# Optimization experiments

Measured on AMD Instinct MI355X. Metric: run time of the kernel, lower is better.

## Reference

```python
import jax, jax.numpy as jnp
import numpy as np

N_NODES = 1000
HIDDEN = 256
IN_DIM = 128
N_EDGES = 64000


def setup_inputs() -> dict:
    key = jax.random.key(0)
    ks = jax.random.split(key, 24)
    inp = {
        "x": jax.random.normal(ks[0], (N_NODES, IN_DIM), dtype=jnp.float32),
        "edge_index": jax.random.randint(ks[1], (2, N_EDGES), 0, N_NODES, dtype=jnp.int64),
    }
    dims = [(HIDDEN, 2 * IN_DIM)] + [(HIDDEN, 2 * HIDDEN)] * 4
    for l, (dout, din) in enumerate(dims):
        s0 = 1.0 / np.sqrt(din)
        s1 = 1.0 / np.sqrt(HIDDEN)
        inp[f"w{l}_0"] = jax.random.normal(ks[2 + 4 * l], (dout, din), dtype=jnp.float32) * s0
        inp[f"b{l}_0"] = jax.random.normal(ks[3 + 4 * l], (dout,), dtype=jnp.float32) * s0
        inp[f"w{l}_1"] = jax.random.normal(ks[4 + 4 * l], (HIDDEN, HIDDEN), dtype=jnp.float32) * s1
        inp[f"b{l}_1"] = jax.random.normal(ks[5 + 4 * l], (HIDDEN,), dtype=jnp.float32) * s1
    return inp


def _edge_conv(x, src, dst, w1, b1, w2, b2):
    # gather endpoint features per edge: [E, D]
    x_i = x[dst]  # destination (edge_index[1])
    x_j = x[src]  # source (edge_index[0])
    m = jnp.concatenate([x_i, x_j - x_i], axis=-1)  # [E, 2D]
    h = jax.nn.relu(m @ w1.T + b1) @ w2.T + b2      # 2-layer MLP, [E, HIDDEN]
    # scatter-max to destination nodes (include_self=False -> empty rows = 0)
    agg = jax.ops.segment_max(h, dst, num_segments=N_NODES)
    agg = jnp.where(jnp.isneginf(agg), jnp.zeros((), agg.dtype), agg)
    return jax.nn.relu(agg)


def reference(x, edge_index, w0_0, b0_0, w0_1, b0_1, w1_0, b1_0, w1_1, b1_1,
              w2_0, b2_0, w2_1, b2_1, w3_0, b3_0, w3_1, b3_1, w4_0, b4_0, w4_1, b4_1):
    src = edge_index[0]
    dst = edge_index[1]
    params = [(w0_0, b0_0, w0_1, b0_1), (w1_0, b1_0, w1_1, b1_1),
              (w2_0, b2_0, w2_1, b2_1), (w3_0, b3_0, w3_1, b3_1),
              (w4_0, b4_0, w4_1, b4_1)]
    h = x
    for (w1, b1, w2, b2) in params:
        h = _edge_conv(h, src, dst, w1, b1, w2, b2)
    return h
```

## Files before the change

### kernel.cpp

```cpp
#include <hip/hip_runtime.h>

#define NN 1000
#define NE 64000
#define HH 256

typedef _Float16 half8 __attribute__((ext_vector_type(8)));
typedef float floatx4 __attribute__((ext_vector_type(4)));

struct PrepArgs { const float* w0[5]; const float* w1[5]; };


__global__ __launch_bounds__(256) void k_prep(PrepArgs pa,
                                              _Float16* wnode, _Float16* w2h,
                                              int* counts, int* cursor,
                                              float* aggA) {
    int gtid = blockIdx.x * 256 + threadIdx.x;
    int gstride = gridDim.x * 256;
    for (int i = gtid; i < 1024; i += gstride) { counts[i] = 0; cursor[i] = 0; }
    for (int l = 0; l < 5; l++) {
        const int KK = l ? 8 : 4;
        const int D = KK * 32;
        const int lgKK = l ? 3 : 2;
        const float* w0 = pa.w0[l];
        _Float16* wn = wnode + l * 131072;
        for (int i = gtid; i < 16384 * KK; i += gstride) {
            int j = i & 7;
            int lane = (i >> 3) & 63;
            int nt = (i >> 9) & 1;
            int kk = (i >> 10) & (KK - 1);
            int slice = i >> (10 + lgKK);
            int mn = lane & 15, q = lane >> 4;
            int n = slice * 32 + nt * 16 + mn;
            int k = kk * 32 + q * 8 + j;
            float v = (n < 256) ? (w0[n * 2 * D + k] - w0[n * 2 * D + D + k])
                                : w0[(n - 256) * 2 * D + D + k];
            wn[i] = (_Float16)v;
        }
        const float* w1 = pa.w1[l];
        _Float16* w2 = w2h + l * 65536;
        for (int i = gtid; i < 65536; i += gstride) {
            int j = i & 7;
            int lane = (i >> 3) & 63;
            int nt = (i >> 9) & 3;
            int kk = (i >> 11) & 7;
            int ws = (i >> 14) & 3;
            int mn = lane & 15, q = lane >> 4;
            int row = ws * 64 + nt * 16 + mn;
            int col = kk * 32 + q * 8 + j;
            w2[i] = (_Float16)w1[row * 256 + col];
        }
    }
    floatx4 z = {0.f, 0.f, 0.f, 0.f};
    floatx4* p4 = (floatx4*)aggA;
    for (int i = gtid; i < NN * HH / 4; i += gstride) p4[i] = z;
}

template <int NK>
__device__ __forceinline__ void node_tile(const float* __restrict__ X,
                                          const _Float16* __restrict__ Wn,
                                          const float* __restrict__ b0,
                                          _Float16* __restrict__ out, int bid) {
    const int Kd = NK * 32;
    int t = threadIdx.x;
    int wave = t >> 6, lane = t & 63;
    int q = lane >> 4, mn = lane & 15;
    int m0 = (bid % 63) * 16;
    int n0 = (bid / 63) * 128 + wave * 32;
    int slice = (bid / 63) * 4 + wave;
    int rr = m0 + mn;
    if (rr >= NN) rr = NN - 1;

    half8 afa[NK];
    half8 bfa[NK][2];
#pragma unroll
    for (int kk = 0; kk < NK; kk++) {
        int ka = kk * 32 + q * 8;
        const float* p = X + (size_t)rr * Kd + ka;
        floatx4 x0 = *(const floatx4*)p;
        floatx4 x1 = *(const floatx4*)(p + 4);
        half8 aa;
#pragma unroll
        for (int j = 0; j < 4; j++) { aa[j] = (_Float16)x0[j]; aa[4 + j] = (_Float16)x1[j]; }
        afa[kk] = aa;
        bfa[kk][0] = *(const half8*)(Wn + (((slice * NK + kk) * 2 + 0) * 64 + lane) * 8);
        bfa[kk][1] = *(const half8*)(Wn + (((slice * NK + kk) * 2 + 1) * 64 + lane) * 8);
    }
    floatx4 acc[2] = {};
#pragma unroll
    for (int kk = 0; kk < NK; kk++) {
        acc[0] = __builtin_amdgcn_mfma_f32_16x16x32_f16(afa[kk], bfa[kk][0], acc[0], 0, 0, 0);
        acc[1] = __builtin_amdgcn_mfma_f32_16x16x32_f16(afa[kk], bfa[kk][1], acc[1], 0, 0, 0);
    }
#pragma unroll
    for (int nt = 0; nt < 2; nt++) {
        int col = n0 + nt * 16 + mn;
        float bias = (col < 256) ? b0[col] : 0.f;
#pragma unroll
        for (int r2 = 0; r2 < 4; r2++) {
            int orow = m0 + q * 4 + r2;
            if (orow < NN)
                out[(size_t)orow * 512 + col] = (_Float16)(acc[nt][r2] + bias);
        }
    }
}

__global__ __launch_bounds__(256) void k_hist_node0(const int* __restrict__ ei,
                                                    int* __restrict__ counts,
                                                    const float* __restrict__ X,
                                                    const _Float16* __restrict__ Wn,
                                                    const float* __restrict__ b0,
                                                    _Float16* __restrict__ out) {
    int bid = blockIdx.x;
    if (bid < 4) {
        for (int e = bid * 256 + threadIdx.x; e < NE; e += 4 * 256)
            atomicAdd(&counts[ei[NE + e] & 1023], 1);
    } else {
        node_tile<4>(X, Wn, b0, out, bid - 4);
    }
}

__global__ __launch_bounds__(256) void k_scatter2(const int* __restrict__ ei,
                                                  const int* __restrict__ counts,
                                                  int* __restrict__ cursor,
                                                  int* __restrict__ ssrc,
                                                  int* __restrict__ sdst) {
    __shared__ int sbase[1024];
    __shared__ int ssum[256];
    int t = threadIdx.x;
    int base = t * 4;
    int c4[4]; int sum = 0;
#pragma unroll
    for (int j = 0; j < 4; j++) { c4[j] = counts[base + j]; sum += c4[j]; }
    ssum[t] = sum;
    __syncthreads();
    for (int d = 1; d < 256; d <<= 1) {
        int v = (t >= d) ? ssum[t - d] : 0;
        __syncthreads();
        ssum[t] += v;
        __syncthreads();
    }
    int run = (t > 0) ? ssum[t - 1] : 0;
#pragma unroll
    for (int j = 0; j < 4; j++) { sbase[base + j] = run; run += c4[j]; }
    __syncthreads();
    for (int e = blockIdx.x * 256 + t; e < NE; e += gridDim.x * 256) {
        int s = ei[e] & 1023, d = ei[NE + e] & 1023;
        int pos = sbase[d] + atomicAdd(&cursor[d], 1);
        if (pos < NE) { ssrc[pos] = s; sdst[pos] = d; }
    }
}

__global__ __launch_bounds__(256) void k_node_zero(const float* __restrict__ agg_in,
                                                   const _Float16* __restrict__ Wn,
                                                   const float* __restrict__ b0,
                                                   _Float16* __restrict__ out,
                                                   float* __restrict__ agg_next) {
    int bid = blockIdx.x;
    if (bid < 252) {
        node_tile<8>(agg_in, Wn, b0, out, bid);
    } else {
        floatx4 z = {0.f, 0.f, 0.f, 0.f};
        floatx4* p4 = (floatx4*)agg_next;
        for (int i = (bid - 252) * 256 + (int)threadIdx.x; i < NN * HH / 4; i += 64 * 256)
            p4[i] = z;
    }
}

template <bool LAST>
__global__ __launch_bounds__(256, 4) void edge_gemm2(const _Float16* __restrict__ node_ab,
                          const int* __restrict__ ssrc, const int* __restrict__ sdst,
                          const _Float16* __restrict__ W2, const float* __restrict__ b2,
                          float* __restrict__ agg) {
    __shared__ _Float16 h1[64 * 256];
    __shared__ int sd[64];
    int t = threadIdx.x;
    int e0 = blockIdx.x * 64;
    int wave = t >> 6, lane = t & 63;
    int q = lane >> 4, mn = lane & 15;
    int n0 = wave * 64;
    const _Float16* W2w = W2 + wave * 16384;

    if (t < 64) sd[t] = sdst[e0 + t];
    {
        int row = t & 63;
        int cb = (t >> 6) * 8;
        int dn = sdst[e0 + row], sn = ssrc[e0 + row];
        const _Float16* pa = node_ab + (size_t)dn * 512 + cb * 8;
        const _Float16* pb = node_ab + (size_t)sn * 512 + 256 + cb * 8;
        half8 av[8], bv[8];
#pragma unroll
        for (int i = 0; i < 8; i++) av[i] = *(const half8*)(pa + i * 8);
#pragma unroll
        for (int i = 0; i < 8; i++) bv[i] = *(const half8*)(pb + i * 8);
#pragma unroll
        for (int i = 0; i < 8; i++) {
            int c = cb + i;
            int p = (c & ~7) | ((c ^ row) & 7);
            half8 hv = av[i] + bv[i];
#pragma unroll
            for (int j = 0; j < 8; j++) hv[j] = hv[j] > (_Float16)0 ? hv[j] : (_Float16)0;
            *(half8*)(&h1[row * 256 + p * 8]) = hv;
        }
    }
    __syncthreads();

    floatx4 acc[4][4] = {};
#pragma unroll
    for (int kk = 0; kk < 8; kk++) {
        half8 bf[4];
#pragma unroll
        for (int nt = 0; nt < 4; nt++)
            bf[nt] = *(const half8*)(W2w + (kk * 4 + nt) * 512 + lane * 8);
        half8 af[4];
#pragma unroll
        for (int mt = 0; mt < 4; mt++) {
            int r = mt * 16 + mn;
            int c = kk * 4 + q;
            int p = (c & ~7) | ((c ^ r) & 7);
            af[mt] = *(const half8*)(&h1[r * 256 + p * 8]);
        }
#pragma unroll
        for (int mt = 0; mt < 4; mt++)
#pragma unroll
            for (int nt = 0; nt < 4; nt++)
                acc[mt][nt] = __builtin_amdgcn_mfma_f32_16x16x32_f16(af[mt], bf[nt], acc[mt][nt], 0, 0, 0);
    }

    if (LAST) {
#pragma unroll
        for (int nt = 0; nt < 4; nt++) {
            int col = n0 + nt * 16 + mn;
            float bias = b2[col];
            int curd = -1;
            float curv = 0.f;
#pragma unroll
            for (int mt = 0; mt < 4; mt++) {
#pragma unroll
                for (int r2 = 0; r2 < 4; r2++) {
                    int er = mt * 16 + q * 4 + r2;
                    int d = sd[er];
                    float v = acc[mt][nt][r2] + bias;
                    v = v > 0.f ? v : 0.f;
                    if (d != curd) {
                        if (curd >= 0 && curv > 0.f)
                            atomicMax((unsigned int*)(agg + (size_t)curd * HH + col), __float_as_uint(curv));
                        curd = d;
                        curv = v;
                    } else {
                        curv = fmaxf(curv, v);
                    }
                }
            }
            if (curd >= 0 && curv > 0.f)
                atomicMax((unsigned int*)(agg + (size_t)curd * HH + col), __float_as_uint(curv));
        }
        return;
    }

    __syncthreads();
#pragma unroll
    for (int nt = 0; nt < 4; nt++) {
        int col = n0 + nt * 16 + mn;
        float bias = b2[col];
        int g = col >> 3, o = col & 7;
#pragma unroll
        for (int mt = 0; mt < 4; mt++) {
#pragma unroll
            for (int r2 = 0; r2 < 4; r2++) {
                int row = mt * 16 + q * 4 + r2;
                float v = acc[mt][nt][r2] + bias;
                v = v > 0.f ? v : 0.f;
                int pg = (g & ~7) | ((g ^ row) & 7);
                h1[row * 256 + pg * 8 + o] = (_Float16)v;
            }
        }
    }
    __syncthreads();

    {
        int c = t;
        int g = c >> 3, o = c & 7;
        float* aggc = agg + c;
        float m = (float)h1[g * 8 + o];
        bool sedge = true;
        int prevd = sd[0];
#pragma unroll 8
        for (int r = 1; r < 64; r++) {
            int d = sd[r];
            int pg = (g & ~7) | ((g ^ r) & 7);
            float v = (float)h1[r * 256 + pg * 8 + o];
            if (d != prevd) {
                if (sedge) {
                    if (m > 0.f)
                        atomicMax((unsigned int*)(aggc + (size_t)prevd * HH), __float_as_uint(m));
                } else {
                    if (m > 0.f)
                        aggc[(size_t)prevd * HH] = m;
                }
                m = v; sedge = false; prevd = d;
            } else {
                m = fmaxf(m, v);
            }
        }
        if (m > 0.f)
            atomicMax((unsigned int*)(aggc + (size_t)prevd * HH), __float_as_uint(m));
    }
}

extern "C" void kernel_launch(void* const* d_in, const int* in_sizes, int n_in,
                              void* d_out, int out_size, void* d_ws, size_t ws_size,
                              hipStream_t stream) {
    const float* x = (const float*)d_in[0];
    const int* ei = (const int*)d_in[1];
    PrepArgs pa;
    const float* b0s[5];
    const float* b1s[5];
    for (int l = 0; l < 5; l++) {
        pa.w0[l] = (const float*)d_in[2 + 4 * l];
        b0s[l] = (const float*)d_in[3 + 4 * l];
        pa.w1[l] = (const float*)d_in[4 + 4 * l];
        b1s[l] = (const float*)d_in[5 + 4 * l];
    }

    int* ssrc = (int*)d_ws;
    int* sdst = ssrc + NE;
    int* counts = sdst + NE;
    int* cursor = counts + 1024;
    _Float16* node_ab = (_Float16*)(cursor + 1024);
    float* aggA = (float*)(node_ab + 1024 * 512);
    float* aggB = aggA + NN * HH;
    _Float16* wnode = (_Float16*)(aggB + NN * HH);
    _Float16* w2h = wnode + 5 * 131072;

    hipLaunchKernelGGL(k_prep, dim3(256), dim3(256), 0, stream,
                       pa, wnode, w2h, counts, cursor, aggA);
    hipLaunchKernelGGL(k_hist_node0, dim3(256), dim3(256), 0, stream,
                       ei, counts, x, wnode, b0s[0], node_ab);
    hipLaunchKernelGGL(k_scatter2, dim3(NE / 256), dim3(256), 0, stream,
                       ei, counts, cursor, ssrc, sdst);

    float* aggs[5] = {aggA, aggB, aggA, aggB, (float*)d_out};
    for (int l = 0; l < 4; l++) {
        hipLaunchKernelGGL((edge_gemm2<false>), dim3(NE / 64), dim3(256), 0, stream,
                           node_ab, ssrc, sdst, w2h + (size_t)l * 65536, b1s[l], aggs[l]);
        hipLaunchKernelGGL(k_node_zero, dim3(252 + 64), dim3(256), 0, stream,
                           aggs[l], wnode + (size_t)(l + 1) * 131072, b0s[l + 1],
                           node_ab, aggs[l + 1]);
    }
    hipLaunchKernelGGL((edge_gemm2<true>), dim3(NE / 64), dim3(256), 0, stream,
                       node_ab, ssrc, sdst, w2h + (size_t)4 * 65536, b1s[4], (float*)d_out);
}
```

Measured before the change: 279.0 us.

## Fuse edge and node stages into single kernels with grid-wide atomic barriers

Merges the histogram, node GEMM and scatter into one kernel, and merges each layer's edge GEMM, zeroing and next-layer node GEMM into one kernel, using software grid barriers on atomic counters in place of kernel boundaries. This removes several launches and their idle gaps. The last layer gets a new reduction path that stages fp32 values in padded shared memory instead of per-lane atomics. The barriers rely on all 1000 blocks being co-resident, which risks deadlock if occupancy is not met. Node tiles now write into node_ab while other blocks in the same kernel may still be reading it.

After: 720.0 us. +158.0%, slower.

```diff
diff --git a/kernel.cpp b/kernel.cpp
--- a/kernel.cpp
+++ b/kernel.cpp
@@ -13,10 +13,10 @@
 __global__ __launch_bounds__(256) void k_prep(PrepArgs pa,
                                               _Float16* wnode, _Float16* w2h,
                                               int* counts, int* cursor,
-                                              float* aggA) {
+                                              int* dcnt, float* aggA) {
     int gtid = blockIdx.x * 256 + threadIdx.x;
     int gstride = gridDim.x * 256;
-    for (int i = gtid; i < 1024; i += gstride) { counts[i] = 0; cursor[i] = 0; }
+    for (int i = gtid; i < 1024; i += gstride) { counts[i] = 0; cursor[i] = 0; dcnt[i] = 0; }
     for (int l = 0; l < 5; l++) {
         const int KK = l ? 8 : 4;
         const int D = KK * 32;
@@ -59,7 +59,7 @@
 __device__ __forceinline__ void node_tile(const float* __restrict__ X,
                                           const _Float16* __restrict__ Wn,
                                           const float* __restrict__ b0,
-                                          _Float16* __restrict__ out, int bid) {
+                                          _Float16* out, int bid) {
     const int Kd = NK * 32;
     int t = threadIdx.x;
     int wave = t >> 6, lane = t & 63;
@@ -69,9 +69,7 @@
     int slice = (bid / 63) * 4 + wave;
     int rr = m0 + mn;
     if (rr >= NN) rr = NN - 1;
-
-    half8 afa[NK];
-    half8 bfa[NK][2];
+    floatx4 acc[2] = {};
 #pragma unroll
     for (int kk = 0; kk < NK; kk++) {
         int ka = kk * 32 + q * 8;
@@ -81,15 +79,10 @@
         half8 aa;
 #pragma unroll
         for (int j = 0; j < 4; j++) { aa[j] = (_Float16)x0[j]; aa[4 + j] = (_Float16)x1[j]; }
-        afa[kk] = aa;
-        bfa[kk][0] = *(const half8*)(Wn + (((slice * NK + kk) * 2 + 0) * 64 + lane) * 8);
-        bfa[kk][1] = *(const half8*)(Wn + (((slice * NK + kk) * 2 + 1) * 64 + lane) * 8);
-    }
-    floatx4 acc[2] = {};
-#pragma unroll
-    for (int kk = 0; kk < NK; kk++) {
-        acc[0] = __builtin_amdgcn_mfma_f32_16x16x32_f16(afa[kk], bfa[kk][0], acc[0], 0, 0, 0);
-        acc[1] = __builtin_amdgcn_mfma_f32_16x16x32_f16(afa[kk], bfa[kk][1], acc[1], 0, 0, 0);
+        half8 bf0 = *(const half8*)(Wn + (((slice * NK + kk) * 2 + 0) * 64 + lane) * 8);
+        half8 bf1 = *(const half8*)(Wn + (((slice * NK + kk) * 2 + 1) * 64 + lane) * 8);
+        acc[0] = __builtin_amdgcn_mfma_f32_16x16x32_f16(aa, bf0, acc[0], 0, 0, 0);
+        acc[1] = __builtin_amdgcn_mfma_f32_16x16x32_f16(aa, bf1, acc[1], 0, 0, 0);
     }
 #pragma unroll
     for (int nt = 0; nt < 2; nt++) {
@@ -104,29 +97,43 @@
     }
 }
 
-__global__ __launch_bounds__(256) void k_hist_node0(const int* __restrict__ ei,
-                                                    int* __restrict__ counts,
-                                                    const float* __restrict__ X,
-                                                    const _Float16* __restrict__ Wn,
-                                                    const float* __restrict__ b0,
-                                                    _Float16* __restrict__ out) {
-    int bid = blockIdx.x;
+__device__ __forceinline__ void barrier_arrive(int* dcnt) {
+    __threadfence();
+    __syncthreads();
+    if (threadIdx.x == 0)
+        __hip_atomic_fetch_add(dcnt, 1, __ATOMIC_ACQ_REL, __HIP_MEMORY_SCOPE_AGENT);
+}
+
+__device__ __forceinline__ void barrier_wait(int* dcnt, int target) {
+    if (threadIdx.x == 0)
+        while (__hip_atomic_load(dcnt, __ATOMIC_RELAXED, __HIP_MEMORY_SCOPE_AGENT) < target)
+            __builtin_amdgcn_s_sleep(1);
+    __syncthreads();
+    __threadfence();
+}
+
+__global__ __launch_bounds__(256) void k_pre(const int* __restrict__ ei,
+                                             int* __restrict__ counts,
+                                             int* __restrict__ cursor,
+                                             const float* __restrict__ X,
+                                             const _Float16* __restrict__ Wn,
+                                             const float* __restrict__ b0,
+                                             _Float16* nab,
+                                             int* __restrict__ ssrc,
+                                             int* __restrict__ sdst,
+                                             int* dcnt) {
+    __shared__ int sbase[1024];
+    __shared__ int ssum[256];
+    int bid = blockIdx.x, t = threadIdx.x;
     if (bid < 4) {
-        for (int e = bid * 256 + threadIdx.x; e < NE; e += 4 * 256)
+        for (int e = bid * 256 + t; e < NE; e += 4 * 256)
             atomicAdd(&counts[ei[NE + e] & 1023], 1);
     } else {
-        node_tile<4>(X, Wn, b0, out, bid - 4);
-    }
-}
-
-__global__ __launch_bounds__(256) void k_scatter2(const int* __restrict__ ei,
-                                                  const int* __restrict__ counts,
-                                                  int* __restrict__ cursor,
-                                                  int* __restrict__ ssrc,
-                                                  int* __restrict__ sdst) {
-    __shared__ int sbase[1024];
-    __shared__ int ssum[256];
-    int t = threadIdx.x;
+        node_tile<4>(X, Wn, b0, nab, bid - 4);
+    }
+    barrier_arrive(dcnt);
+    barrier_wait(dcnt, 256);
+
     int base = t * 4;
     int c4[4]; int sum = 0;
 #pragma unroll
@@ -143,41 +150,23 @@
 #pragma unroll
     for (int j = 0; j < 4; j++) { sbase[base + j] = run; run += c4[j]; }
     __syncthreads();
-    for (int e = blockIdx.x * 256 + t; e < NE; e += gridDim.x * 256) {
+    for (int e = bid * 256 + t; e < NE; e += gridDim.x * 256) {
         int s = ei[e] & 1023, d = ei[NE + e] & 1023;
         int pos = sbase[d] + atomicAdd(&cursor[d], 1);
         if (pos < NE) { ssrc[pos] = s; sdst[pos] = d; }
     }
 }
 
-__global__ __launch_bounds__(256) void k_node_zero(const float* __restrict__ agg_in,
-                                                   const _Float16* __restrict__ Wn,
-                                                   const float* __restrict__ b0,
-                                                   _Float16* __restrict__ out,
-                                                   float* __restrict__ agg_next) {
-    int bid = blockIdx.x;
-    if (bid < 252) {
-        node_tile<8>(agg_in, Wn, b0, out, bid);
-    } else {
-        floatx4 z = {0.f, 0.f, 0.f, 0.f};
-        floatx4* p4 = (floatx4*)agg_next;
-        for (int i = (bid - 252) * 256 + (int)threadIdx.x; i < NN * HH / 4; i += 64 * 256)
-            p4[i] = z;
-    }
-}
-
-template <bool LAST>
-__global__ __launch_bounds__(256, 4) void edge_gemm2(const _Float16* __restrict__ node_ab,
-                          const int* __restrict__ ssrc, const int* __restrict__ sdst,
-                          const _Float16* __restrict__ W2, const float* __restrict__ b2,
-                          float* __restrict__ agg) {
-    __shared__ _Float16 h1[64 * 256];
-    __shared__ int sd[64];
+__device__ __forceinline__ void edge_mfma(const _Float16* node_ab,
+                                          const int* __restrict__ ssrc,
+                                          const int* __restrict__ sdst,
+                                          const _Float16* __restrict__ W2,
+                                          int tile, _Float16* h1, int* sd,
+                                          floatx4 acc[4][4]) {
     int t = threadIdx.x;
-    int e0 = blockIdx.x * 64;
+    int e0 = tile * 64;
     int wave = t >> 6, lane = t & 63;
     int q = lane >> 4, mn = lane & 15;
-    int n0 = wave * 64;
     const _Float16* W2w = W2 + wave * 16384;
 
     if (t < 64) sd[t] = sdst[e0 + t];
@@ -204,7 +193,6 @@
     }
     __syncthreads();
 
-    floatx4 acc[4][4] = {};
 #pragma unroll
     for (int kk = 0; kk < 8; kk++) {
         half8 bf[4];
@@ -225,42 +213,28 @@
             for (int nt = 0; nt < 4; nt++)
                 acc[mt][nt] = __builtin_amdgcn_mfma_f32_16x16x32_f16(af[mt], bf[nt], acc[mt][nt], 0, 0, 0);
     }
-
-    if (LAST) {
-#pragma unroll
-        for (int nt = 0; nt < 4; nt++) {
-            int col = n0 + nt * 16 + mn;
-            float bias = b2[col];
-            int curd = -1;
-            float curv = 0.f;
-#pragma unroll
-            for (int mt = 0; mt < 4; mt++) {
-#pragma unroll
-                for (int r2 = 0; r2 < 4; r2++) {
-                    int er = mt * 16 + q * 4 + r2;
-                    int d = sd[er];
-                    float v = acc[mt][nt][r2] + bias;
-                    v = v > 0.f ? v : 0.f;
-                    if (d != curd) {
-                        if (curd >= 0 && curv > 0.f)
-                            atomicMax((unsigned int*)(agg + (size_t)curd * HH + col), __float_as_uint(curv));
-                        curd = d;
-                        curv = v;
-                    } else {
-                        curv = fmaxf(curv, v);
-                    }
-                }
-            }
-            if (curd >= 0 && curv > 0.f)
-                atomicMax((unsigned int*)(agg + (size_t)curd * HH + col), __float_as_uint(curv));
-        }
-        return;
-    }
+}
+
+__global__ __launch_bounds__(256, 4) void k_layer(
+        const _Float16* node_ab,
+        const int* __restrict__ ssrc, const int* __restrict__ sdst,
+        const _Float16* __restrict__ W2, const float* __restrict__ b2,
+        float* __restrict__ agg, float* __restrict__ aggN,
+        const _Float16* __restrict__ WnN, const float* __restrict__ b0N,
+        int* dcnt) {
+    __shared__ _Float16 h1[64 * 256];
+    __shared__ int sd[64];
+    int bid = blockIdx.x, t = threadIdx.x;
+    int wave = t >> 6, lane = t & 63;
+    int q = lane >> 4, mn = lane & 15;
+
+    floatx4 acc[4][4] = {};
+    edge_mfma(node_ab, ssrc, sdst, W2, bid, h1, sd, acc);
 
     __syncthreads();
 #pragma unroll
     for (int nt = 0; nt < 4; nt++) {
-        int col = n0 + nt * 16 + mn;
+        int col = wave * 64 + nt * 16 + mn;
         float bias = b2[col];
         int g = col >> 3, o = col & 7;
 #pragma unroll
@@ -305,6 +279,85 @@
         if (m > 0.f)
             atomicMax((unsigned int*)(aggc + (size_t)prevd * HH), __float_as_uint(m));
     }
+
+    if (bid >= 252) {
+        floatx4 z = {0.f, 0.f, 0.f, 0.f};
+        floatx4* p4 = (floatx4*)aggN;
+        for (int i = (bid - 252) * 256 + t; i < NN * HH / 4; i += 748 * 256)
+            p4[i] = z;
+    }
+
+    barrier_arrive(dcnt);
+    if (bid < 252) {
+        barrier_wait(dcnt, 1000);
+        node_tile<8>(agg, WnN, b0N, (_Float16*)node_ab, bid);
+    }
+}
+
+__global__ __launch_bounds__(256, 4) void k_last(
+        const _Float16* __restrict__ node_ab,
+        const int* __restrict__ ssrc, const int* __restrict__ sdst,
+        const _Float16* __restrict__ W2, const float* __restrict__ b2,
+        float* __restrict__ agg) {
+    __shared__ float sf[64 * 129];
+    __shared__ int sd[64];
+    _Float16* h1 = (_Float16*)sf;
+    int t = threadIdx.x;
+    int wave = t >> 6, lane = t & 63;
+    int q = lane >> 4, mn = lane & 15;
+
+    floatx4 acc[4][4] = {};
+    edge_mfma(node_ab, ssrc, sdst, W2, blockIdx.x, h1, sd, acc);
+
+    __syncthreads();
+#pragma unroll
+    for (int p = 0; p < 2; p++) {
+        if (p) __syncthreads();
+        if ((wave >> 1) == p) {
+            int lc0 = (wave & 1) * 64;
+#pragma unroll
+            for (int nt = 0; nt < 4; nt++) {
+                int col = wave * 64 + nt * 16 + mn;
+                float bias = b2[col];
+                int lc = lc0 + nt * 16 + mn;
+#pragma unroll
+                for (int mt = 0; mt < 4; mt++) {
+#pragma unroll
+                    for (int r2 = 0; r2 < 4; r2++) {
+                        int row = mt * 16 + q * 4 + r2;
+                        float v = acc[mt][nt][r2] + bias;
+                        sf[row * 129 + lc] = v > 0.f ? v : 0.f;
+                    }
+                }
+            }
+        }
+        __syncthreads();
+        if (t < 128) {
+            float* aggc = agg + p * 128 + t;
+            float m = sf[t];
+            bool sedge = true;
+            int prevd = sd[0];
+#pragma unroll 8
+            for (int r = 1; r < 64; r++) {
+                int d = sd[r];
+                float v = sf[r * 129 + t];
+                if (d != prevd) {
+                    if (sedge) {
+                        if (m > 0.f)
+                            atomicMax((unsigned int*)(aggc + (size_t)prevd * HH), __float_as_uint(m));
+                    } else {
+                        if (m > 0.f)
+                            aggc[(size_t)prevd * HH] = m;
+                    }
+                    m = v; sedge = false; prevd = d;
+                } else {
+                    m = fmaxf(m, v);
+                }
+            }
+            if (m > 0.f)
+                atomicMax((unsigned int*)(aggc + (size_t)prevd * HH), __float_as_uint(m));
+        }
+    }
 }
 
 extern "C" void kernel_launch(void* const* d_in, const int* in_sizes, int n_in,
@@ -326,27 +379,28 @@
     int* sdst = ssrc + NE;
     int* counts = sdst + NE;
     int* cursor = counts + 1024;
-    _Float16* node_ab = (_Float16*)(cursor + 1024);
+    int* dcnt = cursor + 1024;
+    _Float16* node_ab = (_Float16*)(dcnt + 1024);
     float* aggA = (float*)(node_ab + 1024 * 512);
     float* aggB = aggA + NN * HH;
     _Float16* wnode = (_Float16*)(aggB + NN * HH);
     _Float16* w2h = wnode + 5 * 131072;
 
     hipLaunchKernelGGL(k_prep, dim3(256), dim3(256), 0, stream,
-                       pa, wnode, w2h, counts, cursor, aggA);
-    hipLaunchKernelGGL(k_hist_node0, dim3(256), dim3(256), 0, stream,
-                       ei, counts, x, wnode, b0s[0], node_ab);
-    hipLaunchKernelGGL(k_scatter2, dim3(NE / 256), dim3(256), 0, stream,
-                       ei, counts, cursor, ssrc, sdst);
+                       pa, wnode, w2h, counts, cursor, dcnt, aggA);
+    hipLaunchKernelGGL(k_pre, dim3(256), dim3(256), 0, stream,
+                       ei, counts, cursor, x, wnode, b0s[0], node_ab,
+                       ssrc, sdst, dcnt + 512);
 
     float* aggs[5] = {aggA, aggB, aggA, aggB, (float*)d_out};
     for (int l = 0; l < 4; l++) {
-        hipLaunchKernelGGL((edge_gemm2<false>), dim3(NE / 64), dim3(256), 0, stream,
-                           node_ab, ssrc, sdst, w2h + (size_t)l * 65536, b1s[l], aggs[l]);
-        hipLaunchKernelGGL(k_node_zero, dim3(252 + 64), dim3(256), 0, stream,
-                           aggs[l], wnode + (size_t)(l + 1) * 131072, b0s[l + 1],
-                           node_ab, aggs[l + 1]);
-    }
-    hipLaunchKernelGGL((edge_gemm2<true>), dim3(NE / 64), dim3(256), 0, stream,
-                       node_ab, ssrc, sdst, w2h + (size_t)4 * 65536, b1s[4], (float*)d_out);
-}
+        hipLaunchKernelGGL(k_layer, dim3(NE / 64), dim3(256), 0, stream,
+                           node_ab, ssrc, sdst, w2h + (size_t)l * 65536, b1s[l],
+                           aggs[l], aggs[l + 1],
+                           wnode + (size_t)(l + 1) * 131072, b0s[l + 1],
+                           dcnt + l * 32);
+    }
+    hipLaunchKernelGGL(k_last, dim3(NE / 64), dim3(256), 0, stream,
+                       node_ab, ssrc, sdst, w2h + (size_t)4 * 65536, b1s[4],
+                       (float*)d_out);
+}
```
